# Performance work log

Hardware: AMD Instinct MI355X
Metric: run time of the kernel (lower is better)

Reference implementation:

```python
import jax, jax.numpy as jnp
import numpy as np

B, N, L, S, D, H = 16, 8, 64, 32, 256, 128  # 2*H == D required by the module


def _lstm_dir(seq, Wih, Whh, bih, bhh):
    # seq: [T, B, D] -> hidden states [T, B, H]; PyTorch gate order i,f,g,o
    Hd = Whh.shape[1]
    b = seq.shape[1]

    def step(carry, xt):
        h, c = carry
        gates = xt @ Wih.T + h @ Whh.T + bih + bhh  # [B, 4H]
        i, f, g, o = jnp.split(gates, 4, axis=-1)
        c = jax.nn.sigmoid(f) * c + jax.nn.sigmoid(i) * jnp.tanh(g)
        h = jax.nn.sigmoid(o) * jnp.tanh(c)
        return (h, c), h

    init = (jnp.zeros((b, Hd), seq.dtype), jnp.zeros((b, Hd), seq.dtype))
    _, hs = jax.lax.scan(step, init, seq)
    return hs


def setup_inputs() -> dict:
    key = jax.random.key(0)
    ks = jax.random.split(key, 16)
    sc = 1.0 / np.sqrt(D)
    sch = 1.0 / np.sqrt(H)
    inp = {
        "x": jax.random.normal(ks[0], (B, N, L, D), jnp.float32),
        "s": jax.random.normal(ks[1], (B, S, D), jnp.float32),
        # co-attention params (Linear(dim,dim,bias=False) stored [out,in])
        "W": jax.random.normal(ks[2], (D, D), jnp.float32) * sc,
        "U": jax.random.normal(ks[3], (D, D), jnp.float32) * sc,
        "v": jax.random.normal(ks[4], (D,), jnp.float32) * sc,
        # BiLSTM params, forward and backward directions
        "Wih_f": jax.random.normal(ks[5], (4 * H, D), jnp.float32) * sch,
        "Whh_f": jax.random.normal(ks[6], (4 * H, H), jnp.float32) * sch,
        "bih_f": jax.random.normal(ks[7], (4 * H,), jnp.float32) * sch,
        "bhh_f": jax.random.normal(ks[8], (4 * H,), jnp.float32) * sch,
        "Wih_b": jax.random.normal(ks[9], (4 * H, D), jnp.float32) * sch,
        "Whh_b": jax.random.normal(ks[10], (4 * H, H), jnp.float32) * sch,
        "bih_b": jax.random.normal(ks[11], (4 * H,), jnp.float32) * sch,
        "bhh_b": jax.random.normal(ks[12], (4 * H,), jnp.float32) * sch,
        # self-attention params (Linear(D,D) with bias, Linear(D,1) no bias)
        "saW": jax.random.normal(ks[13], (D, D), jnp.float32) * sc,
        "sab": jax.random.normal(ks[14], (D,), jnp.float32) * sc,
        "sav": jax.random.normal(ks[15], (D,), jnp.float32) * sc,
    }
    return inp


def reference(x, s, W, U, v, Wih_f, Whh_f, bih_f, bhh_f,
              Wih_b, Whh_b, bih_b, bhh_b, saW, sab, sav):
    # ---- CoAttention (vectorized over B, N, S) ----
    Wx = jnp.einsum('bnld,ed->bnle', x, W)          # [B,N,L,D]
    Us = jnp.einsum('bsd,ed->bse', s, U)            # [B,S,D]
    # additive attention: tanh(Wx + Us) . v  -> scores over L
    e = jnp.tanh(Wx[:, :, None, :, :] + Us[:, None, :, None, :])  # [B,N,S,L,D]
    scores = jnp.einsum('bnsld,d->bnsl', e, v)      # [B,N,S,L]
    a = jax.nn.softmax(scores, axis=-1)             # softmax over L (dim=0 of [L,B] in torch)
    sr = jnp.einsum('bnsl,bnld->bnsd', a, x)        # [B,N,S,D]
    sr = sr.mean(axis=2)                            # [B,N,D]

    # ---- BiLSTM over the N axis ----
    u = jnp.swapaxes(sr, 0, 1)                      # [N,B,D]
    hf = _lstm_dir(u, Wih_f, Whh_f, bih_f, bhh_f)   # [N,B,H]
    hb = _lstm_dir(u[::-1], Wih_b, Whh_b, bih_b, bhh_b)[::-1]
    c = jnp.swapaxes(jnp.concatenate([hf, hb], axis=-1), 0, 1)  # [B,N,2H]

    # ---- Self-attention pooling ----
    att = jnp.tanh(c @ saW.T + sab) @ sav           # [B,N]
    att = jax.nn.softmax(att, axis=1)
    g = jnp.einsum('bn,bnd->bd', att, c)            # [B,2H]
    return g
```

## Files before the change

kernel.cpp:

```cpp
#include <hip/hip_runtime.h>
#include <cstddef>

#define Bsz 16
#define Nn  8
#define Ll  64
#define Ss  32
#define Dd  256
#define Hh  128

#define LOG2E 1.4426950408889634f

__device__ __forceinline__ float rcp_f(float x)  { return __builtin_amdgcn_rcpf(x); }
__device__ __forceinline__ float exp2_f(float x) { return __builtin_amdgcn_exp2f(x); }

__device__ __forceinline__ float fast_tanh(float x) {
    return 1.0f - 2.0f * rcp_f(exp2_f(x * (2.0f * LOG2E)) + 1.0f);
}
__device__ __forceinline__ float fast_sigmoid(float x) {
    return rcp_f(1.0f + exp2_f(-x * LOG2E));
}
__device__ __forceinline__ float wave_sum(float x) {
#pragma unroll
    for (int off = 32; off > 0; off >>= 1) x += __shfl_xor(x, off, 64);
    return x;
}
__device__ __forceinline__ float wave_max(float x) {
#pragma unroll
    for (int off = 32; off > 0; off >>= 1) x = fmaxf(x, __shfl_xor(x, off, 64));
    return x;
}

__device__ __forceinline__ void gemm_tile_128x64_exp(const float* __restrict__ A,
                                                     const float* __restrict__ B,
                                                     float* __restrict__ C, int ldc,
                                                     float (* __restrict__ As)[44],
                                                     float (* __restrict__ Bs)[44])
{
    const int tid = threadIdx.x;
    const int kq = tid & 7;
    const int mr = tid >> 3;
    const int tx = tid & 15;
    const int ty = tid >> 4;
    float acc[8][4] = {};
    for (int kc = 0; kc < 256; kc += 32) {
#pragma unroll
        for (int p = 0; p < 4; ++p) {
            float4 t = *(const float4*)&A[(size_t)(mr + 32 * p) * 256 + kc + kq * 4];
            *(float4*)&As[mr + 32 * p][kq * 4] = t;
        }
#pragma unroll
        for (int p = 0; p < 2; ++p) {
            float4 t = *(const float4*)&B[(size_t)(mr + 32 * p) * 256 + kc + kq * 4];
            *(float4*)&Bs[mr + 32 * p][kq * 4] = t;
        }
        __syncthreads();
#pragma unroll
        for (int kk = 0; kk < 32; kk += 4) {
            float4 br[4];
#pragma unroll
            for (int j = 0; j < 4; ++j) br[j] = *(const float4*)&Bs[tx + 16 * j][kk];
#pragma unroll
            for (int i = 0; i < 8; ++i) {
                float4 a = *(const float4*)&As[ty + 16 * i][kk];
#pragma unroll
                for (int j = 0; j < 4; ++j) {
                    acc[i][j] = fmaf(a.x, br[j].x, acc[i][j]);
                    acc[i][j] = fmaf(a.y, br[j].y, acc[i][j]);
                    acc[i][j] = fmaf(a.z, br[j].z, acc[i][j]);
                    acc[i][j] = fmaf(a.w, br[j].w, acc[i][j]);
                }
            }
        }
        __syncthreads();
    }
    const float C2 = 2.0f * LOG2E;
#pragma unroll
    for (int i = 0; i < 8; ++i)
#pragma unroll
        for (int j = 0; j < 4; ++j)
            C[(size_t)(ty + 16 * i) * ldc + tx + 16 * j] = exp2_f(acc[i][j] * C2);
}

__global__ __launch_bounds__(256) void gemm_stage1(const float* __restrict__ x,
                                                   const float* __restrict__ s,
                                                   const float* __restrict__ W,
                                                   const float* __restrict__ U,
                                                   float* __restrict__ eWx,
                                                   float* __restrict__ eUs)
{
    __shared__ float As[128][44];
    __shared__ float Bs[64][44];
    int blk = blockIdx.x;
    const float *Ap, *Bp; float* Cp;
    if (blk < 256) {
        int my = blk >> 2, nx = blk & 3;
        Ap = x + (size_t)my * 128 * 256;
        Bp = W + (size_t)nx * 64 * 256;
        Cp = eWx + (size_t)my * 128 * 256 + nx * 64;
    } else {
        int b2 = blk - 256;
        int my = b2 >> 2, nx = b2 & 3;
        Ap = s + (size_t)my * 128 * 256;
        Bp = U + (size_t)nx * 64 * 256;
        Cp = eUs + (size_t)my * 128 * 256 + nx * 64;
    }
    gemm_tile_128x64_exp(Ap, Bp, Cp, 256, As, Bs);
}

__global__ __launch_bounds__(512, 1) void scores_kernel(const float* __restrict__ eWx,
                                                        const float* __restrict__ eUs,
                                                        const float* __restrict__ v,
                                                        float* __restrict__ pabar)
{
    __shared__ float ewx[64][260];
    __shared__ float red[8][64];
    const int bid = blockIdx.x;
    const int bn = bid >> 1, sh = bid & 1;
    const int b = bid >> 4;
    const int tid = threadIdx.x;
    const int lane = tid & 63;
    const int w = __builtin_amdgcn_readfirstlane(tid >> 6);
    {
        const float* wxg = eWx + (size_t)bn * (Ll * Dd);
        int c = tid & 63, r0 = tid >> 6;
#pragma unroll
        for (int p = 0; p < 8; ++p) {
            int r = r0 + p * 8;
            *(float4*)&ewx[r][c * 4] = *(const float4*)&wxg[r * 256 + c * 4];
        }
    }
    __syncthreads();
    const int s0 = sh * 16 + w * 2;
    const float* eu0 = eUs + ((size_t)b * Ss + s0) * 256;
    const float* eu1 = eu0 + 256;
    float acc0 = 0.f, acc1 = 0.f;
#pragma unroll 8
    for (int q = 0; q < 64; ++q) {
        float4 w4 = *(const float4*)&ewx[lane][q * 4];
        float4 e0 = *(const float4*)&eu0[q * 4];
        float4 e1 = *(const float4*)&eu1[q * 4];
        float4 vv = *(const float4*)&v[q * 4];
        acc0 = fmaf(vv.x, rcp_f(fmaf(w4.x, e0.x, 1.0f)), acc0);
        acc0 = fmaf(vv.y, rcp_f(fmaf(w4.y, e0.y, 1.0f)), acc0);
        acc0 = fmaf(vv.z, rcp_f(fmaf(w4.z, e0.z, 1.0f)), acc0);
        acc0 = fmaf(vv.w, rcp_f(fmaf(w4.w, e0.w, 1.0f)), acc0);
        acc1 = fmaf(vv.x, rcp_f(fmaf(w4.x, e1.x, 1.0f)), acc1);
        acc1 = fmaf(vv.y, rcp_f(fmaf(w4.y, e1.y, 1.0f)), acc1);
        acc1 = fmaf(vv.z, rcp_f(fmaf(w4.z, e1.z, 1.0f)), acc1);
        acc1 = fmaf(vv.w, rcp_f(fmaf(w4.w, e1.w, 1.0f)), acc1);
    }
    float t0 = -2.0f * acc0, t1 = -2.0f * acc1;
    float e0 = exp2_f((t0 - wave_max(t0)) * LOG2E);
    float e1 = exp2_f((t1 - wave_max(t1)) * LOG2E);
    float a0 = e0 * rcp_f(wave_sum(e0));
    float a1 = e1 * rcp_f(wave_sum(e1));
    red[w][lane] = a0 + a1;
    __syncthreads();
    if (tid < 64) {
        float p = 0.f;
#pragma unroll
        for (int k = 0; k < 8; ++k) p += red[k][tid];
        pabar[(size_t)bid * 64 + tid] = p;
    }
}

__global__ __launch_bounds__(256) void sr_kernel(const float* __restrict__ pabar,
                                                 const float* __restrict__ x,
                                                 float* __restrict__ sr_out)
{
    int bn = blockIdx.x;
    int tid = threadIdx.x;
    __shared__ float abar[64];
    if (tid < 64)
        abar[tid] = (pabar[(size_t)(bn * 2) * 64 + tid] +
                     pabar[(size_t)(bn * 2 + 1) * 64 + tid]) * (1.0f / 32.0f);
    __syncthreads();
    const float* xp = x + (size_t)bn * Ll * Dd;
    float acc = 0.f;
#pragma unroll 8
    for (int l = 0; l < Ll; ++l)
        acc = fmaf(abar[l], xp[l * Dd + tid], acc);
    sr_out[(size_t)bn * Dd + tid] = acc;
}

__global__ __launch_bounds__(512) void lstm_fused(const float* __restrict__ sr,
                                                  const float* __restrict__ Wih_f,
                                                  const float* __restrict__ Wih_b,
                                                  const float* __restrict__ Whh_f,
                                                  const float* __restrict__ Whh_b,
                                                  const float* __restrict__ bih_f, const float* __restrict__ bhh_f,
                                                  const float* __restrict__ bih_b, const float* __restrict__ bhh_b,
                                                  float* __restrict__ h_out)
{
    int blk = blockIdx.x;
    int dir = blk >> 4, b = blk & 15;
    int g = threadIdx.x;
    __shared__ float s_lds[8][256];
    __shared__ float h[128], c[128], gb[512];
    {
        int nr = g >> 6, off = (g & 63) * 4;
        *(float4*)&s_lds[nr][off] = *(const float4*)&sr[((size_t)b * Nn + nr) * Dd + off];
        if (g < 128) { h[g] = 0.f; c[g] = 0.f; }
    }
    __syncthreads();
    const float* wih = ((dir == 0) ? Wih_f : Wih_b) + (size_t)g * 256;
    const float* srow[8];
#pragma unroll
    for (int tt = 0; tt < 8; ++tt) srow[tt] = s_lds[dir ? 7 - tt : tt];
    float gpre[8] = {};
#pragma unroll
    for (int kq = 0; kq < 64; ++kq) {
        float4 wv = ((const float4*)wih)[kq];
#pragma unroll
        for (int tt = 0; tt < 8; ++tt) {
            const float4 sv = *(const float4*)&srow[tt][kq * 4];
            gpre[tt] = fmaf(wv.x, sv.x, gpre[tt]);
            gpre[tt] = fmaf(wv.y, sv.y, gpre[tt]);
            gpre[tt] = fmaf(wv.z, sv.z, gpre[tt]);
            gpre[tt] = fmaf(wv.w, sv.w, gpre[tt]);
        }
    }
    const float* wr = ((dir == 0) ? Whh_f : Whh_b) + (size_t)g * 128;
    float4 w4[32];
#pragma unroll
    for (int k = 0; k < 32; ++k) w4[k] = ((const float4*)wr)[k];
    float bias = (dir == 0) ? (bih_f[g] + bhh_f[g]) : (bih_b[g] + bhh_b[g]);
    __syncthreads();
#pragma unroll
    for (int t = 0; t < Nn; ++t) {
        float a0 = gpre[t] + bias;
        float a1 = 0.f, a2 = 0.f, a3 = 0.f;
#pragma unroll
        for (int k = 0; k < 32; ++k) {
            float4 hv = *(const float4*)&h[k * 4];
            a0 = fmaf(w4[k].x, hv.x, a0);
            a1 = fmaf(w4[k].y, hv.y, a1);
            a2 = fmaf(w4[k].z, hv.z, a2);
            a3 = fmaf(w4[k].w, hv.w, a3);
        }
        float pre = (a0 + a1) + (a2 + a3);
        float act = (g < 256 || g >= 384) ? fast_sigmoid(pre) : fast_tanh(pre);
        gb[g] = act;
        __syncthreads();
        if (g < 128) {
            float i_ = gb[g], f_ = gb[128 + g], g_ = gb[256 + g], o_ = gb[384 + g];
            float cn = fmaf(f_, c[g], i_ * g_);
            float hn = o_ * fast_tanh(cn);
            c[g] = cn; h[g] = hn;
            int n = dir ? (7 - t) : t;
            h_out[(((size_t)dir * Nn + n) * Bsz + b) * Hh + g] = hn;
        }
        __syncthreads();
    }
}

__global__ __launch_bounds__(256) void attpool_kernel(const float* __restrict__ hbuf,
                                                      const float* __restrict__ saW,
                                                      const float* __restrict__ sab,
                                                      const float* __restrict__ sav,
                                                      float* __restrict__ out)
{
    int b = blockIdx.x;
    int e = threadIdx.x;
    __shared__ float cvec[8][260];
    __shared__ float part[8][4];
#pragma unroll
    for (int n = 0; n < 8; ++n)
        cvec[n][e] = (e < 128) ? hbuf[((size_t)n * Bsz + b) * Hh + e]
                               : hbuf[((size_t)(Nn + n) * Bsz + b) * Hh + (e - 128)];
    __syncthreads();
    const float* wrow = saW + (size_t)e * 256;
    float acc[8];
    float b0 = sab[e];
#pragma unroll
    for (int n = 0; n < 8; ++n) acc[n] = b0;
#pragma unroll 2
    for (int dq0 = 0; dq0 < 8; ++dq0) {
        float4 wq[8];
#pragma unroll
        for (int q = 0; q < 8; ++q) wq[q] = *(const float4*)&wrow[dq0 * 32 + q * 4];
#pragma unroll
        for (int q = 0; q < 8; ++q) {
#pragma unroll
            for (int n = 0; n < 8; ++n) {
                float4 cv = *(const float4*)&cvec[n][dq0 * 32 + q * 4];
                acc[n] = fmaf(wq[q].x, cv.x, acc[n]);
                acc[n] = fmaf(wq[q].y, cv.y, acc[n]);
                acc[n] = fmaf(wq[q].z, cv.z, acc[n]);
                acc[n] = fmaf(wq[q].w, cv.w, acc[n]);
            }
        }
    }
    int w = e >> 6, lane = e & 63;
    float se = sav[e];
#pragma unroll
    for (int n = 0; n < 8; ++n) {
        float t = fast_tanh(acc[n]) * se;
        t = wave_sum(t);
        if (lane == 0) part[n][w] = t;
    }
    __syncthreads();
    float av[8], mx = -1e30f;
#pragma unroll
    for (int n = 0; n < 8; ++n) {
        av[n] = part[n][0] + part[n][1] + part[n][2] + part[n][3];
        mx = fmaxf(mx, av[n]);
    }
    float sum = 0.f;
#pragma unroll
    for (int n = 0; n < 8; ++n) { av[n] = exp2_f((av[n] - mx) * LOG2E); sum += av[n]; }
    float inv = rcp_f(sum);
    float acco = 0.f;
#pragma unroll
    for (int n = 0; n < 8; ++n) acco = fmaf(av[n], cvec[n][e], acco);
    out[b * 256 + e] = acco * inv;
}

extern "C" void kernel_launch(void* const* d_in, const int* in_sizes, int n_in,
                              void* d_out, int out_size, void* d_ws, size_t ws_size,
                              hipStream_t stream) {
    const float* x     = (const float*)d_in[0];
    const float* s     = (const float*)d_in[1];
    const float* W     = (const float*)d_in[2];
    const float* U     = (const float*)d_in[3];
    const float* v     = (const float*)d_in[4];
    const float* Wih_f = (const float*)d_in[5];
    const float* Whh_f = (const float*)d_in[6];
    const float* bih_f = (const float*)d_in[7];
    const float* bhh_f = (const float*)d_in[8];
    const float* Wih_b = (const float*)d_in[9];
    const float* Whh_b = (const float*)d_in[10];
    const float* bih_b = (const float*)d_in[11];
    const float* bhh_b = (const float*)d_in[12];
    const float* saW   = (const float*)d_in[13];
    const float* sab   = (const float*)d_in[14];
    const float* sav   = (const float*)d_in[15];
    float* out = (float*)d_out;
    float* ws  = (float*)d_ws;

    float* eWx   = ws;
    float* eUs   = eWx + 2097152;
    float* pabar = eUs + 131072;
    float* sr_nb = pabar + 16384;
    float* hbuf  = sr_nb + 32768;

    hipLaunchKernelGGL(gemm_stage1, dim3(272), dim3(256), 0, stream, x, s, W, U, eWx, eUs);
    hipLaunchKernelGGL(scores_kernel, dim3(256), dim3(512), 0, stream, eWx, eUs, v, pabar);
    hipLaunchKernelGGL(sr_kernel, dim3(128), dim3(256), 0, stream, pabar, x, sr_nb);
    hipLaunchKernelGGL(lstm_fused, dim3(32), dim3(512), 0, stream,
                       sr_nb, Wih_f, Wih_b, Whh_f, Whh_b,
                       bih_f, bhh_f, bih_b, bhh_b, hbuf);
    hipLaunchKernelGGL(attpool_kernel, dim3(16), dim3(256), 0, stream, hbuf, saW, sab, sav, out);
}
```

Baseline: 190.1 us.

## Replace FP32 SIMT projection GEMM with split-bf16 MFMA GEMM

Adds a pre-pass that splits x, s, W and U into high and low bf16 halves. The projection GEMM then runs on bf16 MFMA instructions using three products (hi*hi, hi*lo, lo*hi) to approximate fp32 accuracy, replacing the scalar FMA tiled GEMM. The aim is to cut the arithmetic cost of the largest GEMM by using the matrix cores. In exchange it adds an extra kernel launch, extra global traffic for the split copies, more workspace, fewer blocks (136 vs 272), and slightly lower precision.

```diff
diff --git a/kernel.cpp b/kernel.cpp
--- a/kernel.cpp
+++ b/kernel.cpp
@@ -10,6 +10,9 @@
 
 #define LOG2E 1.4426950408889634f
 
+typedef short bf16x8 __attribute__((ext_vector_type(8)));
+typedef float f32x4  __attribute__((ext_vector_type(4)));
+
 __device__ __forceinline__ float rcp_f(float x)  { return __builtin_amdgcn_rcpf(x); }
 __device__ __forceinline__ float exp2_f(float x) { return __builtin_amdgcn_exp2f(x); }
 
@@ -30,81 +33,106 @@
     return x;
 }
 
-__device__ __forceinline__ void gemm_tile_128x64_exp(const float* __restrict__ A,
-                                                     const float* __restrict__ B,
-                                                     float* __restrict__ C, int ldc,
-                                                     float (* __restrict__ As)[44],
-                                                     float (* __restrict__ Bs)[44])
-{
+__device__ __forceinline__ void bsplit(float f, unsigned short& h, unsigned short& l) {
+    unsigned u  = __builtin_bit_cast(unsigned, f);
+    unsigned hb = (u + 0x7FFFu + ((u >> 16) & 1u)) >> 16;
+    float hf = __builtin_bit_cast(float, hb << 16);
+    h = (unsigned short)hb;
+    float r = f - hf;
+    unsigned ur = __builtin_bit_cast(unsigned, r);
+    l = (unsigned short)((ur + 0x7FFFu + ((ur >> 16) & 1u)) >> 16);
+}
+
+__global__ __launch_bounds__(256) void split_bf16(
+    const float* __restrict__ x, const float* __restrict__ s,
+    const float* __restrict__ W, const float* __restrict__ U,
+    unsigned short* __restrict__ xh, unsigned short* __restrict__ xl,
+    unsigned short* __restrict__ sh2, unsigned short* __restrict__ sl2,
+    unsigned short* __restrict__ Wh, unsigned short* __restrict__ Wl,
+    unsigned short* __restrict__ Uh, unsigned short* __restrict__ Ul)
+{
+    int g = blockIdx.x * 256 + threadIdx.x;
+    const float* src; unsigned short *dh, *dl; int e;
+    if      (g < 524288) { src = x; dh = xh;  dl = xl;  e = g; }
+    else if (g < 557056) { src = s; dh = sh2; dl = sl2; e = g - 524288; }
+    else if (g < 573440) { src = W; dh = Wh;  dl = Wl;  e = g - 557056; }
+    else                 { src = U; dh = Uh;  dl = Ul;  e = g - 573440; }
+    float4 f = ((const float4*)src)[e];
+    ushort4 h, l;
+    bsplit(f.x, h.x, l.x);
+    bsplit(f.y, h.y, l.y);
+    bsplit(f.z, h.z, l.z);
+    bsplit(f.w, h.w, l.w);
+    ((ushort4*)dh)[e] = h;
+    ((ushort4*)dl)[e] = l;
+}
+
+__global__ __launch_bounds__(256) void gemm_mfma(
+    const unsigned short* __restrict__ xh, const unsigned short* __restrict__ xl,
+    const unsigned short* __restrict__ sh2, const unsigned short* __restrict__ sl2,
+    const unsigned short* __restrict__ Wh, const unsigned short* __restrict__ Wl,
+    const unsigned short* __restrict__ Uh, const unsigned short* __restrict__ Ul,
+    float* __restrict__ eWx, float* __restrict__ eUs)
+{
+    __shared__ unsigned short Ah[128][40], Al[128][40], Bh[128][40], Bl[128][40];
     const int tid = threadIdx.x;
-    const int kq = tid & 7;
-    const int mr = tid >> 3;
-    const int tx = tid & 15;
-    const int ty = tid >> 4;
-    float acc[8][4] = {};
+    int blk = blockIdx.x;
+    const unsigned short *agh, *agl, *bgh, *bgl; float* C;
+    if (blk < 128) {
+        int my = blk >> 1, nxb = blk & 1;
+        agh = xh + (size_t)my * 128 * 256;  agl = xl + (size_t)my * 128 * 256;
+        bgh = Wh + (size_t)nxb * 128 * 256; bgl = Wl + (size_t)nxb * 128 * 256;
+        C = eWx + (size_t)my * 128 * 256 + nxb * 128;
+    } else {
+        int b2 = blk - 128;
+        int my = b2 >> 1, nxb = b2 & 1;
+        agh = sh2 + (size_t)my * 128 * 256; agl = sl2 + (size_t)my * 128 * 256;
+        bgh = Uh + (size_t)nxb * 128 * 256; bgl = Ul + (size_t)nxb * 128 * 256;
+        C = eUs + (size_t)my * 128 * 256 + nxb * 128;
+    }
+    const int lane = tid & 63, w = tid >> 6;
+    const int wm = (w & 1) * 64, wn = (w >> 1) * 64;
+    const int fr = lane & 15, fk = (lane >> 4) * 8;
+    f32x4 acc[4][4] = {};
     for (int kc = 0; kc < 256; kc += 32) {
 #pragma unroll
-        for (int p = 0; p < 4; ++p) {
-            float4 t = *(const float4*)&A[(size_t)(mr + 32 * p) * 256 + kc + kq * 4];
-            *(float4*)&As[mr + 32 * p][kq * 4] = t;
-        }
-#pragma unroll
         for (int p = 0; p < 2; ++p) {
-            float4 t = *(const float4*)&B[(size_t)(mr + 32 * p) * 256 + kc + kq * 4];
-            *(float4*)&Bs[mr + 32 * p][kq * 4] = t;
+            int idx = p * 256 + tid;
+            int row = idx >> 2, ch = (idx & 3) * 8;
+            *(uint4*)&Ah[row][ch] = *(const uint4*)&agh[(size_t)row * 256 + kc + ch];
+            *(uint4*)&Al[row][ch] = *(const uint4*)&agl[(size_t)row * 256 + kc + ch];
+            *(uint4*)&Bh[row][ch] = *(const uint4*)&bgh[(size_t)row * 256 + kc + ch];
+            *(uint4*)&Bl[row][ch] = *(const uint4*)&bgl[(size_t)row * 256 + kc + ch];
         }
         __syncthreads();
-#pragma unroll
-        for (int kk = 0; kk < 32; kk += 4) {
-            float4 br[4];
-#pragma unroll
-            for (int j = 0; j < 4; ++j) br[j] = *(const float4*)&Bs[tx + 16 * j][kk];
-#pragma unroll
-            for (int i = 0; i < 8; ++i) {
-                float4 a = *(const float4*)&As[ty + 16 * i][kk];
-#pragma unroll
-                for (int j = 0; j < 4; ++j) {
-                    acc[i][j] = fmaf(a.x, br[j].x, acc[i][j]);
-                    acc[i][j] = fmaf(a.y, br[j].y, acc[i][j]);
-                    acc[i][j] = fmaf(a.z, br[j].z, acc[i][j]);
-                    acc[i][j] = fmaf(a.w, br[j].w, acc[i][j]);
-                }
+        bf16x8 ah4[4], al4[4], bh4[4], bl4[4];
+#pragma unroll
+        for (int i = 0; i < 4; ++i) {
+            ah4[i] = *(const bf16x8*)&Ah[wm + 16 * i + fr][fk];
+            al4[i] = *(const bf16x8*)&Al[wm + 16 * i + fr][fk];
+            bh4[i] = *(const bf16x8*)&Bh[wn + 16 * i + fr][fk];
+            bl4[i] = *(const bf16x8*)&Bl[wn + 16 * i + fr][fk];
+        }
+#pragma unroll
+        for (int i = 0; i < 4; ++i)
+#pragma unroll
+            for (int j = 0; j < 4; ++j) {
+                acc[i][j] = __builtin_amdgcn_mfma_f32_16x16x32_bf16(ah4[i], bh4[j], acc[i][j], 0, 0, 0);
+                acc[i][j] = __builtin_amdgcn_mfma_f32_16x16x32_bf16(ah4[i], bl4[j], acc[i][j], 0, 0, 0);
+                acc[i][j] = __builtin_amdgcn_mfma_f32_16x16x32_bf16(al4[i], bh4[j], acc[i][j], 0, 0, 0);
             }
-        }
         __syncthreads();
     }
     const float C2 = 2.0f * LOG2E;
-#pragma unroll
-    for (int i = 0; i < 8; ++i)
+    const int crow = (lane >> 4) * 4, ccol = lane & 15;
+#pragma unroll
+    for (int i = 0; i < 4; ++i)
 #pragma unroll
         for (int j = 0; j < 4; ++j)
-            C[(size_t)(ty + 16 * i) * ldc + tx + 16 * j] = exp2_f(acc[i][j] * C2);
-}
-
-__global__ __launch_bounds__(256) void gemm_stage1(const float* __restrict__ x,
-                                                   const float* __restrict__ s,
-                                                   const float* __restrict__ W,
-                                                   const float* __restrict__ U,
-                                                   float* __restrict__ eWx,
-                                                   float* __restrict__ eUs)
-{
-    __shared__ float As[128][44];
-    __shared__ float Bs[64][44];
-    int blk = blockIdx.x;
-    const float *Ap, *Bp; float* Cp;
-    if (blk < 256) {
-        int my = blk >> 2, nx = blk & 3;
-        Ap = x + (size_t)my * 128 * 256;
-        Bp = W + (size_t)nx * 64 * 256;
-        Cp = eWx + (size_t)my * 128 * 256 + nx * 64;
-    } else {
-        int b2 = blk - 256;
-        int my = b2 >> 2, nx = b2 & 3;
-        Ap = s + (size_t)my * 128 * 256;
-        Bp = U + (size_t)nx * 64 * 256;
-        Cp = eUs + (size_t)my * 128 * 256 + nx * 64;
-    }
-    gemm_tile_128x64_exp(Ap, Bp, Cp, 256, As, Bs);
+#pragma unroll
+            for (int r = 0; r < 4; ++r)
+                C[(size_t)(wm + 16 * i + crow + r) * 256 + wn + 16 * j + ccol] =
+                    exp2_f(acc[i][j][r] * C2);
 }
 
 __global__ __launch_bounds__(512, 1) void scores_kernel(const float* __restrict__ eWx,
@@ -343,8 +371,20 @@
     float* pabar = eUs + 131072;
     float* sr_nb = pabar + 16384;
     float* hbuf  = sr_nb + 32768;
-
-    hipLaunchKernelGGL(gemm_stage1, dim3(272), dim3(256), 0, stream, x, s, W, U, eWx, eUs);
+    unsigned short* us_base = (unsigned short*)(hbuf + 32768);
+    unsigned short* xh  = us_base;
+    unsigned short* xl  = xh  + 2097152;
+    unsigned short* sh2 = xl  + 2097152;
+    unsigned short* sl2 = sh2 + 131072;
+    unsigned short* Wh  = sl2 + 131072;
+    unsigned short* Wl  = Wh  + 65536;
+    unsigned short* Uh  = Wl  + 65536;
+    unsigned short* Ul  = Uh  + 65536;
+
+    hipLaunchKernelGGL(split_bf16, dim3(2304), dim3(256), 0, stream,
+                       x, s, W, U, xh, xl, sh2, sl2, Wh, Wl, Uh, Ul);
+    hipLaunchKernelGGL(gemm_mfma, dim3(136), dim3(256), 0, stream,
+                       xh, xl, sh2, sl2, Wh, Wl, Uh, Ul, eWx, eUs);
     hipLaunchKernelGGL(scores_kernel, dim3(256), dim3(512), 0, stream, eWx, eUs, v, pabar);
     hipLaunchKernelGGL(sr_kernel, dim3(128), dim3(256), 0, stream, pabar, x, sr_nb);
     hipLaunchKernelGGL(lstm_fused, dim3(32), dim3(512), 0, stream,
```

New measurement: 173.4 us. 1.1x faster.
